# Kernel optimization log

Hardware: AMD Instinct MI355X
Metric: run time of the kernel (lower is better)

Reference implementation:

```python
import jax, jax.numpy as jnp
import numpy as np

N = 20000; DEG = 32; E = N * DEG; F = 142; D = 32; H = 4; HD = H * D; C = 2
_BN = np.float32(1.0 / np.sqrt(1.0 + 1e-5))  # eval-mode BatchNorm1d with running mean 0 / var 1


def _prelu(x, a):
    return jnp.where(x >= 0, x, a * x)


def _layernorm(x, g, b):
    m = x.mean(-1, keepdims=True)
    v = x.var(-1, keepdims=True)
    return (x - m) / jnp.sqrt(v + 1e-5) * g + b


def _conv(h, src, dst, Wq, bq, Wk, bk, Wv, bv, Ws, bs, Wg, bg, lng, lnb, a):
    # TransformerConv: u_dot_v attention (q from src, k from dst), edge softmax over
    # incoming edges of each dst node, u_mul_e + sum aggregation, gated skip, LN, PReLU.
    n = h.shape[0]
    q = (h @ Wq + bq).reshape(n, H, D)
    k = (h @ Wk + bk).reshape(n, H, D)
    v = (h @ Wv + bv).reshape(n, H, D)
    scores = jnp.einsum('ehd,ehd->eh', q[src], k[dst]) / np.float32(np.sqrt(D))  # [E,H]
    m = jax.ops.segment_max(scores, dst, num_segments=n)
    p = jnp.exp(scores - m[dst])
    s = jax.ops.segment_sum(p, dst, num_segments=n)
    sa = p / s[dst]                                                              # [E,H]
    agg = jax.ops.segment_sum(v[src] * sa[..., None], dst, num_segments=n)       # [N,H,D]
    agg = agg.reshape(n, HD)
    skip = h @ Ws + bs
    g = jax.nn.sigmoid(jnp.concatenate([skip, agg, skip - agg], -1) @ Wg + bg)
    rst = g * skip + (1.0 - g) * agg
    return _prelu(_layernorm(rst, lng, lnb), a)


def setup_inputs() -> dict:
    ks = jax.random.split(jax.random.key(0), 64)
    def nrm(i, shape, s=0.05):
        return (jax.random.normal(ks[i], shape) * s).astype(jnp.float32)
    inp = {}
    inp['features'] = jax.random.normal(ks[0], (N, F), jnp.float32)
    inp['label_emb'] = nrm(1, (C + 1, F)).at[C].set(0.0)  # padding_idx = n_classes
    inp['W1'] = nrm(2, (F, HD)); inp['b1'] = jnp.zeros(HD)
    inp['W2'] = nrm(3, (F, HD)); inp['b2'] = jnp.zeros(HD)
    inp['bn0_g'] = jnp.ones(HD); inp['bn0_b'] = jnp.zeros(HD)
    inp['a3'] = 0.25 * jnp.ones(1)
    inp['W3'] = nrm(4, (HD, F)); inp['b3'] = jnp.zeros(F)
    i = 5
    for l, fin in enumerate([F, HD]):
        inp[f'Wq{l}'] = nrm(i, (fin, HD)); i += 1
        inp[f'bq{l}'] = jnp.zeros(HD)
        inp[f'Wk{l}'] = nrm(i, (fin, HD)); i += 1
        inp[f'bk{l}'] = jnp.zeros(HD)
        inp[f'Wv{l}'] = nrm(i, (fin, HD)); i += 1
        inp[f'bv{l}'] = jnp.zeros(HD)
        inp[f'Ws{l}'] = nrm(i, (fin, HD)); i += 1
        inp[f'bs{l}'] = jnp.zeros(HD)
        inp[f'Wg{l}'] = nrm(i, (3 * HD, 1)); i += 1
        inp[f'bg{l}'] = jnp.zeros(1)
        inp[f'ln{l}_g'] = jnp.ones(HD)
        inp[f'ln{l}_b'] = jnp.zeros(HD)
    inp['a_conv'] = 0.25 * jnp.ones(1)  # single PReLU instance shared by both conv layers
    inp['W4'] = nrm(i, (HD, HD)); i += 1; inp['b4'] = jnp.zeros(HD)
    inp['bn1_g'] = jnp.ones(HD); inp['bn1_b'] = jnp.zeros(HD)
    inp['a5'] = 0.25 * jnp.ones(1)
    inp['W5'] = nrm(i, (HD, C)); i += 1; inp['b5'] = jnp.zeros(C)
    inp['labels'] = jax.random.randint(ks[40], (N,), 0, C + 1)
    inp['edge_src'] = jax.random.randint(ks[41], (E,), 0, N)
    inp['edge_dst'] = jnp.repeat(jnp.arange(N), DEG)  # every node has in-degree DEG
    return inp


def reference(features, label_emb, W1, b1, W2, b2, bn0_g, bn0_b, a3, W3, b3,
              Wq0, bq0, Wk0, bk0, Wv0, bv0, Ws0, bs0, Wg0, bg0, ln0_g, ln0_b,
              Wq1, bq1, Wk1, bk1, Wv1, bv1, Ws1, bs1, Wg1, bg1, ln1_g, ln1_b,
              a_conv, W4, b4, bn1_g, bn1_b, a5, W5, b5,
              labels, edge_src, edge_dst):
    le = label_emb[labels]                                   # [N,F]
    le = features @ W1 + b1 + le @ W2 + b2                   # [N,HD]
    le = _prelu(le * _BN * bn0_g + bn0_b, a3) @ W3 + b3      # BN -> PReLU -> Linear
    h = features + le
    h = _conv(h, edge_src, edge_dst, Wq0, bq0, Wk0, bk0, Wv0, bv0, Ws0, bs0, Wg0, bg0, ln0_g, ln0_b, a_conv)
    h = _conv(h, edge_src, edge_dst, Wq1, bq1, Wk1, bk1, Wv1, bv1, Ws1, bs1, Wg1, bg1, ln1_g, ln1_b, a_conv)
    x = h @ W4 + b4
    x = _prelu(x * _BN * bn1_g + bn1_b, a5)
    return x @ W5 + b5                                       # [N, n_classes]
```

## Files before the change

kernel.cpp:

```cpp
#include <hip/hip_runtime.h>
#include <math.h>

#define N_NODES 20000
#define DEG 32
#define F_IN 142
#define HD 128
#define NHEAD 4
#define DHEAD 32
#define N_CLS 2

#define BN_SCALE 0.9999950000374997f
#define INV_SQRT_D 0.17677669529663687f

typedef short v8s __attribute__((ext_vector_type(8)));
typedef float v4f __attribute__((ext_vector_type(4)));

__device__ __forceinline__ unsigned short f2bf(float f) {
    unsigned u = __float_as_uint(f);
    return (unsigned short)((u + 0x7fffu + ((u >> 16) & 1u)) >> 16);
}
__device__ __forceinline__ unsigned pack2bf(float a, float b) {
    return (unsigned)f2bf(a) | ((unsigned)f2bf(b) << 16);
}
__device__ __forceinline__ float bf2f(unsigned short s) {
    return __uint_as_float((unsigned)s << 16);
}
__device__ __forceinline__ float bflo(unsigned u) { return __uint_as_float(u << 16); }
__device__ __forceinline__ float bfhi(unsigned u) { return __uint_as_float(u & 0xffff0000u); }

__device__ __forceinline__ v8s pack8(float4 f0, float4 f1) {
    union { v8s s; unsigned u[4]; } x;
    x.u[0] = pack2bf(f0.x, f0.y);
    x.u[1] = pack2bf(f0.z, f0.w);
    x.u[2] = pack2bf(f1.x, f1.y);
    x.u[3] = pack2bf(f1.z, f1.w);
    return x.s;
}

__device__ __forceinline__ void swizTile(const float* __restrict__ W, int K, int KC,
                                         int tile, int L, short* __restrict__ outBase) {
    const int kc = tile % KC, nt = tile / KC;
    const int n = nt * 16 + (L & 15);
    const int kb = kc * 32 + (L >> 4) * 8;
    short v[8] __attribute__((aligned(16)));
    #pragma unroll
    for (int j = 0; j < 8; ++j) {
        int k = kb + j;
        v[j] = (k < K) ? (short)f2bf(W[(size_t)k * HD + n]) : (short)0;
    }
    *(uint4*)(outBase + ((size_t)tile * 64 + L) * 8) = *(const uint4*)v;
}

__global__ __launch_bounds__(128) void kPrep(
        const float* W142a, const float* W142b, const float* W142c,
        const float* W142d, const float* W142e,
        const float* W128a, const float* W128b, const float* W128c,
        const float* W128d, const float* W128e,
        const float* __restrict__ W3,
        const float* __restrict__ lemb, const float* __restrict__ W2,
        const float* __restrict__ b1, const float* __restrict__ b2,
        short* __restrict__ Wf142, short* __restrict__ Wf128,
        short* __restrict__ W3f, float* __restrict__ E) {
    const int b = blockIdx.x;
    const int t = threadIdx.x;
    if (b < 100) {
        const float* Wt[5] = {W142a, W142b, W142c, W142d, W142e};
        const int idx = b * 2 + (t >> 6);
        const int mat = idx / 40, tile = idx - mat * 40;
        swizTile(Wt[mat], F_IN, 5, tile, t & 63, Wf142 + (size_t)mat * 20480);
    } else if (b < 180) {
        const float* Wt[5] = {W128a, W128b, W128c, W128d, W128e};
        const int idx = (b - 100) * 2 + (t >> 6);
        const int mat = idx >> 5, tile = idx & 31;
        swizTile(Wt[mat], HD, 4, tile, t & 63, Wf128 + (size_t)mat * 16384);
    } else if (b < 198) {
        const int tile = (b - 180) * 2 + (t >> 6);
        const int kc = tile & 3, nt = tile >> 2;
        const int L = t & 63;
        const int n = nt * 16 + (L & 15);
        const int kb = kc * 32 + (L >> 4) * 8;
        short v[8] __attribute__((aligned(16)));
        #pragma unroll
        for (int j = 0; j < 8; ++j)
            v[j] = (n < F_IN) ? (short)f2bf(W3[(size_t)(kb + j) * F_IN + n]) : (short)0;
        *(uint4*)(W3f + ((size_t)tile * 64 + L) * 8) = *(const uint4*)v;
    } else {
        __shared__ float sl[F_IN];
        const int l = b - 198;
        for (int f = t; f < F_IN; f += 128) sl[f] = lemb[l * F_IN + f];
        __syncthreads();
        float acc = b1[t] + b2[t];
        for (int f = 0; f < F_IN; ++f) acc += sl[f] * W2[f * HD + t];
        E[l * HD + t] = acc;
    }
}

__global__ __launch_bounds__(256) void kAB_m(const float* __restrict__ feat,
        const short* __restrict__ W1f, const short* __restrict__ W3f,
        const int* __restrict__ labels, const float* __restrict__ E,
        const float* __restrict__ bng, const float* __restrict__ bnb,
        const float* __restrict__ a3, const float* __restrict__ b3,
        float* __restrict__ h) {
    __shared__ float4 sAv[32 * 164 / 4];
    __shared__ uint4  sTv[32 * 136 / 8];
    __shared__ int sLab[32];
    float* sA = (float*)sAv;
    unsigned short* sT = (unsigned short*)sTv;
    const int tid = threadIdx.x;
    const int row0 = blockIdx.x * 32;
    for (int idx = tid; idx < 32 * F_IN; idx += 256) {
        int r = idx / F_IN, c = idx - r * F_IN;
        sA[r * 164 + c] = feat[(size_t)(row0 + r) * F_IN + c];
    }
    {   const int ZC = 160 - F_IN;
        for (int idx = tid; idx < 32 * ZC; idx += 256) {
            int r = idx / ZC, c = idx - r * ZC;
            sA[r * 164 + F_IN + c] = 0.f;
        }
    }
    if (tid < 32) sLab[tid] = labels[row0 + tid];
    __syncthreads();

    const int lane = tid & 63, w = tid >> 6;
    const int m = lane & 15, q = lane >> 4;
    const int nt0 = w * 2, nt1 = nt0 + 1;

    v4f acc00 = {0.f,0.f,0.f,0.f}, acc01 = acc00, acc10 = acc00, acc11 = acc00;
    #pragma unroll
    for (int kc = 0; kc < 5; ++kc) {
        const float* r0 = sA + m * 164 + kc * 32 + q * 8;
        const float* r1 = sA + (16 + m) * 164 + kc * 32 + q * 8;
        v8s a0 = pack8(*(const float4*)r0, *(const float4*)(r0 + 4));
        v8s a1 = pack8(*(const float4*)r1, *(const float4*)(r1 + 4));
        v8s b0 = *(const v8s*)(W1f + ((size_t)((nt0 * 5 + kc) * 64 + lane)) * 8);
        v8s b1 = *(const v8s*)(W1f + ((size_t)((nt1 * 5 + kc) * 64 + lane)) * 8);
        acc00 = __builtin_amdgcn_mfma_f32_16x16x32_bf16(a0, b0, acc00, 0, 0, 0);
        acc01 = __builtin_amdgcn_mfma_f32_16x16x32_bf16(a0, b1, acc01, 0, 0, 0);
        acc10 = __builtin_amdgcn_mfma_f32_16x16x32_bf16(a1, b0, acc10, 0, 0, 0);
        acc11 = __builtin_amdgcn_mfma_f32_16x16x32_bf16(a1, b1, acc11, 0, 0, 0);
    }
    const int c0 = w * 32 + m, c1 = c0 + 16;
    {
        const float g0 = bng[c0] * BN_SCALE, g1 = bng[c1] * BN_SCALE;
        const float bb0 = bnb[c0], bb1 = bnb[c1];
        const float al = a3[0];
        #pragma unroll
        for (int rt = 0; rt < 2; ++rt) {
            v4f A0 = rt ? acc10 : acc00;
            v4f A1 = rt ? acc11 : acc01;
            #pragma unroll
            for (int i = 0; i < 4; ++i) {
                const int r = rt * 16 + q * 4 + i;
                const int lab = sLab[r];
                float y0 = (A0[i] + E[lab * HD + c0]) * g0 + bb0;
                float y1 = (A1[i] + E[lab * HD + c1]) * g1 + bb1;
                y0 = (y0 >= 0.f) ? y0 : al * y0;
                y1 = (y1 >= 0.f) ? y1 : al * y1;
                sT[r * 136 + c0] = f2bf(y0);
                sT[r * 136 + c1] = f2bf(y1);
            }
        }
    }
    __syncthreads();

    v4f d00 = {0.f,0.f,0.f,0.f}, d01 = d00, d10 = d00, d11 = d00, e0 = d00, e1 = d00;
    #pragma unroll
    for (int kc = 0; kc < 4; ++kc) {
        v8s a0 = *(const v8s*)(sT + m * 136 + kc * 32 + q * 8);
        v8s a1 = *(const v8s*)(sT + (16 + m) * 136 + kc * 32 + q * 8);
        v8s b0 = *(const v8s*)(W3f + ((size_t)((nt0 * 4 + kc) * 64 + lane)) * 8);
        v8s b1 = *(const v8s*)(W3f + ((size_t)((nt1 * 4 + kc) * 64 + lane)) * 8);
        d00 = __builtin_amdgcn_mfma_f32_16x16x32_bf16(a0, b0, d00, 0, 0, 0);
        d01 = __builtin_amdgcn_mfma_f32_16x16x32_bf16(a0, b1, d01, 0, 0, 0);
        d10 = __builtin_amdgcn_mfma_f32_16x16x32_bf16(a1, b0, d10, 0, 0, 0);
        d11 = __builtin_amdgcn_mfma_f32_16x16x32_bf16(a1, b1, d11, 0, 0, 0);
        if (w == 3) {
            v8s b2 = *(const v8s*)(W3f + ((size_t)((8 * 4 + kc) * 64 + lane)) * 8);
            e0 = __builtin_amdgcn_mfma_f32_16x16x32_bf16(a0, b2, e0, 0, 0, 0);
            e1 = __builtin_amdgcn_mfma_f32_16x16x32_bf16(a1, b2, e1, 0, 0, 0);
        }
    }
    const float b30 = b3[c0], b31 = b3[c1];
    #pragma unroll
    for (int rt = 0; rt < 2; ++rt) {
        v4f D0 = rt ? d10 : d00;
        v4f D1 = rt ? d11 : d01;
        #pragma unroll
        for (int i = 0; i < 4; ++i) {
            const int r = row0 + rt * 16 + q * 4 + i;
            h[(size_t)r * F_IN + c0] = feat[(size_t)r * F_IN + c0] + D0[i] + b30;
            h[(size_t)r * F_IN + c1] = feat[(size_t)r * F_IN + c1] + D1[i] + b31;
        }
    }
    if (w == 3) {
        const int c2 = 128 + m;
        if (c2 < F_IN) {
            const float b32 = b3[c2];
            #pragma unroll
            for (int i = 0; i < 4; ++i) {
                const int ra = row0 + q * 4 + i;
                const int rb = ra + 16;
                h[(size_t)ra * F_IN + c2] = feat[(size_t)ra * F_IN + c2] + e0[i] + b32;
                h[(size_t)rb * F_IN + c2] = feat[(size_t)rb * F_IN + c2] + e1[i] + b32;
            }
        }
    }
}

template<int K, int LDSK, int KC>
__global__ __launch_bounds__(256) void kC4_mf(const float* __restrict__ A,
        const short* __restrict__ WfBase,
        const float* __restrict__ bq, const float* __restrict__ bk,
        const float* __restrict__ bv, const float* __restrict__ bs,
        unsigned short* __restrict__ qh, unsigned short* __restrict__ kh,
        unsigned short* __restrict__ vh, float* __restrict__ sOut) {
    __shared__ float4 sAv[32 * LDSK / 4];
    float* sA = (float*)sAv;
    const int tid = threadIdx.x;
    const int row0 = blockIdx.x * 32;
    for (int idx = tid; idx < 32 * K; idx += 256) {
        int r = idx / K, c = idx - r * K;
        sA[r * LDSK + c] = A[(size_t)(row0 + r) * K + c];
    }
    if (K < KC * 32) {
        const int ZC = KC * 32 - K;
        for (int idx = tid; idx < 32 * ZC; idx += 256) {
            int r = idx / ZC, c = idx - r * ZC;
            sA[r * LDSK + K + c] = 0.f;
        }
    }
    __syncthreads();

    const int lane = tid & 63, w = tid >> 6;
    const int m = lane & 15, q = lane >> 4;
    const int nt0 = w * 2, nt1 = nt0 + 1;

    v8s afr0[KC], afr1[KC];
    #pragma unroll
    for (int kc = 0; kc < KC; ++kc) {
        const float* r0 = sA + m * LDSK + kc * 32 + q * 8;
        const float* r1 = sA + (16 + m) * LDSK + kc * 32 + q * 8;
        afr0[kc] = pack8(*(const float4*)r0, *(const float4*)(r0 + 4));
        afr1[kc] = pack8(*(const float4*)r1, *(const float4*)(r1 + 4));
    }

    const int c0 = w * 32 + m, c1 = c0 + 16;
    #pragma unroll
    for (int mat = 0; mat < 4; ++mat) {
        const short* Wf = WfBase + (size_t)mat * (KC * 4096);
        const float* bias = (mat == 0) ? bq : (mat == 1) ? bk : (mat == 2) ? bv : bs;
        v4f acc00 = {0.f,0.f,0.f,0.f}, acc01 = acc00, acc10 = acc00, acc11 = acc00;
        #pragma unroll
        for (int kc = 0; kc < KC; ++kc) {
            v8s b0 = *(const v8s*)(Wf + ((size_t)((nt0 * KC + kc) * 64 + lane)) * 8);
            v8s b1 = *(const v8s*)(Wf + ((size_t)((nt1 * KC + kc) * 64 + lane)) * 8);
            acc00 = __builtin_amdgcn_mfma_f32_16x16x32_bf16(afr0[kc], b0, acc00, 0, 0, 0);
            acc01 = __builtin_amdgcn_mfma_f32_16x16x32_bf16(afr0[kc], b1, acc01, 0, 0, 0);
            acc10 = __builtin_amdgcn_mfma_f32_16x16x32_bf16(afr1[kc], b0, acc10, 0, 0, 0);
            acc11 = __builtin_amdgcn_mfma_f32_16x16x32_bf16(afr1[kc], b1, acc11, 0, 0, 0);
        }
        const float b0v = bias[c0], b1v = bias[c1];
        if (mat < 3) {
            unsigned short* outh = (mat == 0) ? qh : (mat == 1) ? kh : vh;
            unsigned short* outw = outh + ((size_t)w * N_NODES + row0) * DHEAD;
            #pragma unroll
            for (int rt = 0; rt < 2; ++rt) {
                v4f A0 = rt ? acc10 : acc00;
                v4f A1 = rt ? acc11 : acc01;
                #pragma unroll
                for (int i = 0; i < 4; ++i) {
                    const int r = rt * 16 + q * 4 + i;
                    outw[(size_t)r * DHEAD + m]      = f2bf(A0[i] + b0v);
                    outw[(size_t)r * DHEAD + 16 + m] = f2bf(A1[i] + b1v);
                }
            }
        } else {
            #pragma unroll
            for (int rt = 0; rt < 2; ++rt) {
                v4f A0 = rt ? acc10 : acc00;
                v4f A1 = rt ? acc11 : acc01;
                #pragma unroll
                for (int i = 0; i < 4; ++i) {
                    const int r = rt * 16 + q * 4 + i;
                    sOut[(size_t)(row0 + r) * HD + c0] = A0[i] + b0v;
                    sOut[(size_t)(row0 + r) * HD + c1] = A1[i] + b1v;
                }
            }
        }
    }
}

__global__ __launch_bounds__(256) void kD_h(const unsigned short* __restrict__ qh,
        const unsigned short* __restrict__ kh, const unsigned short* __restrict__ vh,
        const int* __restrict__ esrc, float* __restrict__ agg) {
    __shared__ float sk[8][DHEAD];
    __shared__ int ssrc[8][DEG];
    __shared__ float sa[8][DEG];
    const int h = blockIdx.y;
    const int n0 = blockIdx.x * 8;
    const int t = threadIdx.x;
    const int j = t >> 5, e = t & 31;

    ssrc[j][e] = esrc[n0 * DEG + t];
    if (t < 128) {
        unsigned u = *((const unsigned*)(kh + ((size_t)h * N_NODES + n0) * DHEAD) + t);
        float* skf = &sk[0][0];
        skf[2 * t]     = bflo(u);
        skf[2 * t + 1] = bfhi(u);
    }
    __syncthreads();

    const int src = ssrc[j][e];
    const uint4* qp = (const uint4*)(qh + ((size_t)h * N_NODES + src) * DHEAD);
    const float* kj = sk[j];
    float sc = 0.f;
    #pragma unroll
    for (int i = 0; i < 4; ++i) {
        uint4 u = qp[i];
        sc = fmaf(bflo(u.x), kj[i * 8 + 0], sc);
        sc = fmaf(bfhi(u.x), kj[i * 8 + 1], sc);
        sc = fmaf(bflo(u.y), kj[i * 8 + 2], sc);
        sc = fmaf(bfhi(u.y), kj[i * 8 + 3], sc);
        sc = fmaf(bflo(u.z), kj[i * 8 + 4], sc);
        sc = fmaf(bfhi(u.z), kj[i * 8 + 5], sc);
        sc = fmaf(bflo(u.w), kj[i * 8 + 6], sc);
        sc = fmaf(bfhi(u.w), kj[i * 8 + 7], sc);
    }
    sc *= INV_SQRT_D;
    float m = sc;
    #pragma unroll
    for (int off = 16; off > 0; off >>= 1)
        m = fmaxf(m, __shfl_xor(m, off, 32));
    float p = expf(sc - m);
    float ssum = p;
    #pragma unroll
    for (int off = 16; off > 0; off >>= 1)
        ssum += __shfl_xor(ssum, off, 32);
    sa[j][e] = p / ssum;
    __syncthreads();

    const int d = t & 31;
    const unsigned short* vbase = vh + (size_t)h * N_NODES * DHEAD + d;
    float acc = 0.f;
    #pragma unroll
    for (int e2 = 0; e2 < DEG; ++e2) {
        const int s2 = ssrc[j][e2];
        acc = fmaf(bf2f(vbase[(size_t)s2 * DHEAD]), sa[j][e2], acc);
    }
    agg[(size_t)(n0 + j) * HD + h * DHEAD + d] = acc;
}

__device__ __forceinline__ float blockSum128(float v, float* s2, int tid) {
    #pragma unroll
    for (int o = 32; o > 0; o >>= 1) v += __shfl_xor(v, o, 64);
    if ((tid & 63) == 0) s2[tid >> 6] = v;
    __syncthreads();
    float r = s2[0] + s2[1];
    __syncthreads();
    return r;
}

__global__ void kE(const float* __restrict__ skip, const float* __restrict__ agg,
                   const float* __restrict__ Wg, const float* __restrict__ bg,
                   const float* __restrict__ lng, const float* __restrict__ lnb,
                   const float* __restrict__ ac,
                   float* __restrict__ hout) {
    __shared__ float red[2];
    int n = blockIdx.x, c = threadIdx.x;
    float sk = skip[n * HD + c], ag = agg[n * HD + c];
    float part = sk * Wg[c] + ag * Wg[HD + c] + (sk - ag) * Wg[2 * HD + c];
    float z = blockSum128(part, red, c) + bg[0];
    float g = 1.f / (1.f + expf(-z));
    float r = g * sk + (1.f - g) * ag;
    float mean = blockSum128(r, red, c) * (1.f / HD);
    float dv = r - mean;
    float var = blockSum128(dv * dv, red, c) * (1.f / HD);
    float y = dv * rsqrtf(var + 1e-5f) * lng[c] + lnb[c];
    float a = ac[0];
    hout[n * HD + c] = (y >= 0.f) ? y : a * y;
}

__global__ __launch_bounds__(256) void kF_mf2(const float* __restrict__ A,
        const short* __restrict__ W4f, const float* __restrict__ b4,
        const float* __restrict__ bng, const float* __restrict__ bnb,
        const float* __restrict__ a5, const float* __restrict__ W5,
        const float* __restrict__ b5, float* __restrict__ out) {
    __shared__ float4 sAv[32 * 132 / 4];
    float* sA = (float*)sAv;
    const int tid = threadIdx.x;
    const int row0 = blockIdx.x * 32;
    for (int idx = tid; idx < 32 * HD; idx += 256) {
        int r = idx >> 7, c = idx & 127;
        sA[r * 132 + c] = A[(size_t)(row0 + r) * HD + c];
    }
    __syncthreads();
    const int lane = tid & 63, w = tid >> 6;
    const int m = lane & 15, q = lane >> 4;
    const int nt0 = w * 2, nt1 = nt0 + 1;
    v4f acc00 = {0.f,0.f,0.f,0.f}, acc01 = acc00, acc10 = acc00, acc11 = acc00;
    #pragma unroll
    for (int kc = 0; kc < 4; ++kc) {
        const float* r0 = sA + m * 132 + kc * 32 + q * 8;
        const float* r1 = sA + (16 + m) * 132 + kc * 32 + q * 8;
        v8s a0 = pack8(*(const float4*)r0, *(const float4*)(r0 + 4));
        v8s a1 = pack8(*(const float4*)r1, *(const float4*)(r1 + 4));
        v8s b0 = *(const v8s*)(W4f + ((size_t)((nt0 * 4 + kc) * 64 + lane)) * 8);
        v8s b1 = *(const v8s*)(W4f + ((size_t)((nt1 * 4 + kc) * 64 + lane)) * 8);
        acc00 = __builtin_amdgcn_mfma_f32_16x16x32_bf16(a0, b0, acc00, 0, 0, 0);
        acc01 = __builtin_amdgcn_mfma_f32_16x16x32_bf16(a0, b1, acc01, 0, 0, 0);
        acc10 = __builtin_amdgcn_mfma_f32_16x16x32_bf16(a1, b0, acc10, 0, 0, 0);
        acc11 = __builtin_amdgcn_mfma_f32_16x16x32_bf16(a1, b1, acc11, 0, 0, 0);
    }
    __syncthreads();
    const int c0 = w * 32 + m, c1 = c0 + 16;
    const float g0 = bng[c0] * BN_SCALE, g1 = bng[c1] * BN_SCALE;
    const float bb0 = bnb[c0], bb1 = bnb[c1];
    const float b40 = b4[c0], b41 = b4[c1];
    const float al = a5[0];
    #pragma unroll
    for (int rt = 0; rt < 2; ++rt) {
        v4f A0 = rt ? acc10 : acc00;
        v4f A1 = rt ? acc11 : acc01;
        #pragma unroll
        for (int i = 0; i < 4; ++i) {
            const int r = rt * 16 + q * 4 + i;
            float y0 = (A0[i] + b40) * g0 + bb0;
            float y1 = (A1[i] + b41) * g1 + bb1;
            y0 = (y0 >= 0.f) ? y0 : al * y0;
            y1 = (y1 >= 0.f) ? y1 : al * y1;
            sA[r * 132 + c0] = y0;
            sA[r * 132 + c1] = y1;
        }
    }
    __syncthreads();
    if (tid < 64) {
        const int r = tid >> 1, cls = tid & 1;
        const float* yr = sA + r * 132;
        float s = b5[cls];
        #pragma unroll 8
        for (int c = 0; c < HD; ++c)
            s = fmaf(yr[c], W5[c * 2 + cls], s);
        out[(size_t)(row0 + r) * N_CLS + cls] = s;
    }
}

extern "C" void kernel_launch(void* const* d_in, const int* in_sizes, int n_in,
                              void* d_out, int out_size, void* d_ws, size_t ws_size,
                              hipStream_t stream) {
    const float* feat  = (const float*)d_in[0];
    const float* lemb  = (const float*)d_in[1];
    const float* W1    = (const float*)d_in[2];
    const float* b1    = (const float*)d_in[3];
    const float* W2    = (const float*)d_in[4];
    const float* b2    = (const float*)d_in[5];
    const float* bn0g  = (const float*)d_in[6];
    const float* bn0b  = (const float*)d_in[7];
    const float* a3    = (const float*)d_in[8];
    const float* W3    = (const float*)d_in[9];
    const float* b3    = (const float*)d_in[10];
    const float* aconv = (const float*)d_in[35];
    const float* W4    = (const float*)d_in[36];
    const float* b4    = (const float*)d_in[37];
    const float* bn1g  = (const float*)d_in[38];
    const float* bn1b  = (const float*)d_in[39];
    const float* a5    = (const float*)d_in[40];
    const float* W5    = (const float*)d_in[41];
    const float* b5    = (const float*)d_in[42];
    const int*   labels = (const int*)d_in[43];
    const int*   esrc   = (const int*)d_in[44];

    char* ws = (char*)d_ws;
    float* bh  = (float*)ws;                       ws += sizeof(float) * N_NODES * F_IN;
    float* bs  = (float*)ws;                       ws += sizeof(float) * N_NODES * HD;
    float* bag = (float*)ws;                       ws += sizeof(float) * N_NODES * HD;
    float* bh2 = (float*)ws;                       ws += sizeof(float) * N_NODES * HD;
    unsigned short* bqh = (unsigned short*)ws;     ws += sizeof(short) * N_NODES * HD;
    unsigned short* bkh = (unsigned short*)ws;     ws += sizeof(short) * N_NODES * HD;
    unsigned short* bvh = (unsigned short*)ws;     ws += sizeof(short) * N_NODES * HD;
    short* Wf142 = (short*)ws;                     ws += sizeof(short) * 5 * 20480;
    short* Wf128 = (short*)ws;                     ws += sizeof(short) * 5 * 16384;
    short* W3f = (short*)ws;                       ws += sizeof(short) * 36 * 512;
    float* bE  = (float*)ws;                       ws += sizeof(float) * 3 * HD;
    float* out = (float*)d_out;

    dim3 gT(N_NODES / 32);
    dim3 gD(N_NODES / 8, NHEAD);

    kPrep<<<dim3(201), 128, 0, stream>>>(
        W1, (const float*)d_in[11], (const float*)d_in[13],
        (const float*)d_in[15], (const float*)d_in[17],
        (const float*)d_in[23], (const float*)d_in[25],
        (const float*)d_in[27], (const float*)d_in[29], W4,
        W3, lemb, W2, b1, b2,
        Wf142, Wf128, W3f, bE);

    kAB_m<<<gT, 256, 0, stream>>>(feat, Wf142, W3f, labels, bE, bn0g, bn0b, a3, b3, bh);

    kC4_mf<F_IN, 164, 5><<<gT, 256, 0, stream>>>(bh, Wf142 + 20480,
        (const float*)d_in[12], (const float*)d_in[14],
        (const float*)d_in[16], (const float*)d_in[18],
        bqh, bkh, bvh, bs);
    kD_h<<<gD, 256, 0, stream>>>(bqh, bkh, bvh, esrc, bag);
    kE<<<dim3(N_NODES), HD, 0, stream>>>(bs, bag, (const float*)d_in[19], (const float*)d_in[20],
        (const float*)d_in[21], (const float*)d_in[22], aconv, bh2);

    kC4_mf<HD, 132, 4><<<gT, 256, 0, stream>>>(bh2, Wf128,
        (const float*)d_in[24], (const float*)d_in[26],
        (const float*)d_in[28], (const float*)d_in[30],
        bqh, bkh, bvh, bs);
    kD_h<<<gD, 256, 0, stream>>>(bqh, bkh, bvh, esrc, bag);
    kE<<<dim3(N_NODES), HD, 0, stream>>>(bs, bag, (const float*)d_in[31], (const float*)d_in[32],
        (const float*)d_in[33], (const float*)d_in[34], aconv, bh2);

    kF_mf2<<<gT, 256, 0, stream>>>(bh2, Wf128 + 4 * 16384, b4, bn1g, bn1b, a5, W5, b5, out);
}
```

Before: 313.7 us.

## Fuse input MLP with first QKV projection and gate/LN into following GEMMs

```diff
diff --git a/kernel.cpp b/kernel.cpp
--- a/kernel.cpp
+++ b/kernel.cpp
@@ -95,17 +95,22 @@
     }
 }
 
-__global__ __launch_bounds__(256) void kAB_m(const float* __restrict__ feat,
-        const short* __restrict__ W1f, const short* __restrict__ W3f,
+__global__ __launch_bounds__(256) void kABC(const float* __restrict__ feat,
+        const short* __restrict__ Wf142, const short* __restrict__ W3f,
         const int* __restrict__ labels, const float* __restrict__ E,
         const float* __restrict__ bng, const float* __restrict__ bnb,
         const float* __restrict__ a3, const float* __restrict__ b3,
-        float* __restrict__ h) {
+        const float* __restrict__ bq, const float* __restrict__ bk,
+        const float* __restrict__ bv, const float* __restrict__ bsb,
+        unsigned short* __restrict__ qh, unsigned short* __restrict__ kh,
+        unsigned short* __restrict__ vh, float* __restrict__ sOut) {
     __shared__ float4 sAv[32 * 164 / 4];
     __shared__ uint4  sTv[32 * 136 / 8];
+    __shared__ uint4  sHv[32 * 168 / 8];
     __shared__ int sLab[32];
     float* sA = (float*)sAv;
     unsigned short* sT = (unsigned short*)sTv;
+    unsigned short* sH = (unsigned short*)sHv;
     const int tid = threadIdx.x;
     const int row0 = blockIdx.x * 32;
     for (int idx = tid; idx < 32 * F_IN; idx += 256) {
@@ -124,23 +129,23 @@
     const int lane = tid & 63, w = tid >> 6;
     const int m = lane & 15, q = lane >> 4;
     const int nt0 = w * 2, nt1 = nt0 + 1;
-
-    v4f acc00 = {0.f,0.f,0.f,0.f}, acc01 = acc00, acc10 = acc00, acc11 = acc00;
-    #pragma unroll
-    for (int kc = 0; kc < 5; ++kc) {
-        const float* r0 = sA + m * 164 + kc * 32 + q * 8;
-        const float* r1 = sA + (16 + m) * 164 + kc * 32 + q * 8;
-        v8s a0 = pack8(*(const float4*)r0, *(const float4*)(r0 + 4));
-        v8s a1 = pack8(*(const float4*)r1, *(const float4*)(r1 + 4));
-        v8s b0 = *(const v8s*)(W1f + ((size_t)((nt0 * 5 + kc) * 64 + lane)) * 8);
-        v8s b1 = *(const v8s*)(W1f + ((size_t)((nt1 * 5 + kc) * 64 + lane)) * 8);
-        acc00 = __builtin_amdgcn_mfma_f32_16x16x32_bf16(a0, b0, acc00, 0, 0, 0);
-        acc01 = __builtin_amdgcn_mfma_f32_16x16x32_bf16(a0, b1, acc01, 0, 0, 0);
-        acc10 = __builtin_amdgcn_mfma_f32_16x16x32_bf16(a1, b0, acc10, 0, 0, 0);
-        acc11 = __builtin_amdgcn_mfma_f32_16x16x32_bf16(a1, b1, acc11, 0, 0, 0);
-    }
     const int c0 = w * 32 + m, c1 = c0 + 16;
+
     {
+        v4f acc00 = {0.f,0.f,0.f,0.f}, acc01 = acc00, acc10 = acc00, acc11 = acc00;
+        #pragma unroll
+        for (int kc = 0; kc < 5; ++kc) {
+            const float* r0 = sA + m * 164 + kc * 32 + q * 8;
+            const float* r1 = sA + (16 + m) * 164 + kc * 32 + q * 8;
+            v8s a0 = pack8(*(const float4*)r0, *(const float4*)(r0 + 4));
+            v8s a1 = pack8(*(const float4*)r1, *(const float4*)(r1 + 4));
+            v8s b0 = *(const v8s*)(Wf142 + ((size_t)((nt0 * 5 + kc) * 64 + lane)) * 8);
+            v8s b1 = *(const v8s*)(Wf142 + ((size_t)((nt1 * 5 + kc) * 64 + lane)) * 8);
+            acc00 = __builtin_amdgcn_mfma_f32_16x16x32_bf16(a0, b0, acc00, 0, 0, 0);
+            acc01 = __builtin_amdgcn_mfma_f32_16x16x32_bf16(a0, b1, acc01, 0, 0, 0);
+            acc10 = __builtin_amdgcn_mfma_f32_16x16x32_bf16(a1, b0, acc10, 0, 0, 0);
+            acc11 = __builtin_amdgcn_mfma_f32_16x16x32_bf16(a1, b1, acc11, 0, 0, 0);
+        }
         const float g0 = bng[c0] * BN_SCALE, g1 = bng[c1] * BN_SCALE;
         const float bb0 = bnb[c0], bb1 = bnb[c1];
         const float al = a3[0];
@@ -163,97 +168,197 @@
     }
     __syncthreads();
 
-    v4f d00 = {0.f,0.f,0.f,0.f}, d01 = d00, d10 = d00, d11 = d00, e0 = d00, e1 = d00;
-    #pragma unroll
-    for (int kc = 0; kc < 4; ++kc) {
-        v8s a0 = *(const v8s*)(sT + m * 136 + kc * 32 + q * 8);
-        v8s a1 = *(const v8s*)(sT + (16 + m) * 136 + kc * 32 + q * 8);
-        v8s b0 = *(const v8s*)(W3f + ((size_t)((nt0 * 4 + kc) * 64 + lane)) * 8);
-        v8s b1 = *(const v8s*)(W3f + ((size_t)((nt1 * 4 + kc) * 64 + lane)) * 8);
-        d00 = __builtin_amdgcn_mfma_f32_16x16x32_bf16(a0, b0, d00, 0, 0, 0);
-        d01 = __builtin_amdgcn_mfma_f32_16x16x32_bf16(a0, b1, d01, 0, 0, 0);
-        d10 = __builtin_amdgcn_mfma_f32_16x16x32_bf16(a1, b0, d10, 0, 0, 0);
-        d11 = __builtin_amdgcn_mfma_f32_16x16x32_bf16(a1, b1, d11, 0, 0, 0);
+    {
+        v4f d00 = {0.f,0.f,0.f,0.f}, d01 = d00, d10 = d00, d11 = d00, e0 = d00, e1 = d00;
+        #pragma unroll
+        for (int kc = 0; kc < 4; ++kc) {
+            v8s a0 = *(const v8s*)(sT + m * 136 + kc * 32 + q * 8);
+            v8s a1 = *(const v8s*)(sT + (16 + m) * 136 + kc * 32 + q * 8);
+            v8s b0 = *(const v8s*)(W3f + ((size_t)((nt0 * 4 + kc) * 64 + lane)) * 8);
+            v8s b1 = *(const v8s*)(W3f + ((size_t)((nt1 * 4 + kc) * 64 + lane)) * 8);
+            d00 = __builtin_amdgcn_mfma_f32_16x16x32_bf16(a0, b0, d00, 0, 0, 0);
+            d01 = __builtin_amdgcn_mfma_f32_16x16x32_bf16(a0, b1, d01, 0, 0, 0);
+            d10 = __builtin_amdgcn_mfma_f32_16x16x32_bf16(a1, b0, d10, 0, 0, 0);
+            d11 = __builtin_amdgcn_mfma_f32_16x16x32_bf16(a1, b1, d11, 0, 0, 0);
+            if (w == 3) {
+                v8s b2 = *(const v8s*)(W3f + ((size_t)((8 * 4 + kc) * 64 + lane)) * 8);
+                e0 = __builtin_amdgcn_mfma_f32_16x16x32_bf16(a0, b2, e0, 0, 0, 0);
+                e1 = __builtin_amdgcn_mfma_f32_16x16x32_bf16(a1, b2, e1, 0, 0, 0);
+            }
+        }
+        const float b30 = b3[c0], b31 = b3[c1];
+        #pragma unroll
+        for (int rt = 0; rt < 2; ++rt) {
+            v4f D0 = rt ? d10 : d00;
+            v4f D1 = rt ? d11 : d01;
+            #pragma unroll
+            for (int i = 0; i < 4; ++i) {
+                const int r = rt * 16 + q * 4 + i;
+                sH[r * 168 + c0] = f2bf(sA[r * 164 + c0] + D0[i] + b30);
+                sH[r * 168 + c1] = f2bf(sA[r * 164 + c1] + D1[i] + b31);
+            }
+        }
         if (w == 3) {
-            v8s b2 = *(const v8s*)(W3f + ((size_t)((8 * 4 + kc) * 64 + lane)) * 8);
-            e0 = __builtin_amdgcn_mfma_f32_16x16x32_bf16(a0, b2, e0, 0, 0, 0);
-            e1 = __builtin_amdgcn_mfma_f32_16x16x32_bf16(a1, b2, e1, 0, 0, 0);
-        }
-    }
-    const float b30 = b3[c0], b31 = b3[c1];
-    #pragma unroll
-    for (int rt = 0; rt < 2; ++rt) {
-        v4f D0 = rt ? d10 : d00;
-        v4f D1 = rt ? d11 : d01;
-        #pragma unroll
-        for (int i = 0; i < 4; ++i) {
-            const int r = row0 + rt * 16 + q * 4 + i;
-            h[(size_t)r * F_IN + c0] = feat[(size_t)r * F_IN + c0] + D0[i] + b30;
-            h[(size_t)r * F_IN + c1] = feat[(size_t)r * F_IN + c1] + D1[i] + b31;
-        }
-    }
-    if (w == 3) {
-        const int c2 = 128 + m;
-        if (c2 < F_IN) {
-            const float b32 = b3[c2];
+            const int c2 = 128 + m;
+            const bool ok = (c2 < F_IN);
+            const float b32 = ok ? b3[c2] : 0.f;
             #pragma unroll
             for (int i = 0; i < 4; ++i) {
-                const int ra = row0 + q * 4 + i;
+                const int ra = q * 4 + i;
                 const int rb = ra + 16;
-                h[(size_t)ra * F_IN + c2] = feat[(size_t)ra * F_IN + c2] + e0[i] + b32;
-                h[(size_t)rb * F_IN + c2] = feat[(size_t)rb * F_IN + c2] + e1[i] + b32;
-            }
-        }
-    }
-}
-
-template<int K, int LDSK, int KC>
-__global__ __launch_bounds__(256) void kC4_mf(const float* __restrict__ A,
-        const short* __restrict__ WfBase,
+                sH[ra * 168 + c2] = ok ? f2bf(sA[ra * 164 + c2] + e0[i] + b32) : (unsigned short)0;
+                sH[rb * 168 + c2] = ok ? f2bf(sA[rb * 164 + c2] + e1[i] + b32) : (unsigned short)0;
+            }
+        }
+        if (tid < 256) {
+            const int r = tid >> 3, cp = tid & 7;
+            ((unsigned*)sH)[r * 84 + 72 + cp] = 0u;
+        }
+    }
+    __syncthreads();
+
+    v8s afr0[5], afr1[5];
+    #pragma unroll
+    for (int kc = 0; kc < 5; ++kc) {
+        afr0[kc] = *(const v8s*)(sH + m * 168 + kc * 32 + q * 8);
+        afr1[kc] = *(const v8s*)(sH + (16 + m) * 168 + kc * 32 + q * 8);
+    }
+    #pragma unroll
+    for (int mat = 0; mat < 4; ++mat) {
+        const short* Wf = Wf142 + (size_t)(mat + 1) * 20480;
+        const float* bias = (mat == 0) ? bq : (mat == 1) ? bk : (mat == 2) ? bv : bsb;
+        v4f acc00 = {0.f,0.f,0.f,0.f}, acc01 = acc00, acc10 = acc00, acc11 = acc00;
+        #pragma unroll
+        for (int kc = 0; kc < 5; ++kc) {
+            v8s b0 = *(const v8s*)(Wf + ((size_t)((nt0 * 5 + kc) * 64 + lane)) * 8);
+            v8s b1 = *(const v8s*)(Wf + ((size_t)((nt1 * 5 + kc) * 64 + lane)) * 8);
+            acc00 = __builtin_amdgcn_mfma_f32_16x16x32_bf16(afr0[kc], b0, acc00, 0, 0, 0);
+            acc01 = __builtin_amdgcn_mfma_f32_16x16x32_bf16(afr0[kc], b1, acc01, 0, 0, 0);
+            acc10 = __builtin_amdgcn_mfma_f32_16x16x32_bf16(afr1[kc], b0, acc10, 0, 0, 0);
+            acc11 = __builtin_amdgcn_mfma_f32_16x16x32_bf16(afr1[kc], b1, acc11, 0, 0, 0);
+        }
+        const float b0v = bias[c0], b1v = bias[c1];
+        if (mat < 3) {
+            unsigned short* outh = (mat == 0) ? qh : (mat == 1) ? kh : vh;
+            unsigned short* outw = outh + ((size_t)w * N_NODES + row0) * DHEAD;
+            #pragma unroll
+            for (int rt = 0; rt < 2; ++rt) {
+                v4f A0 = rt ? acc10 : acc00;
+                v4f A1 = rt ? acc11 : acc01;
+                #pragma unroll
+                for (int i = 0; i < 4; ++i) {
+                    const int r = rt * 16 + q * 4 + i;
+                    outw[(size_t)r * DHEAD + m]      = f2bf(A0[i] + b0v);
+                    outw[(size_t)r * DHEAD + 16 + m] = f2bf(A1[i] + b1v);
+                }
+            }
+        } else {
+            #pragma unroll
+            for (int rt = 0; rt < 2; ++rt) {
+                v4f A0 = rt ? acc10 : acc00;
+                v4f A1 = rt ? acc11 : acc01;
+                #pragma unroll
+                for (int i = 0; i < 4; ++i) {
+                    const int r = rt * 16 + q * 4 + i;
+                    sOut[(size_t)(row0 + r) * HD + c0] = A0[i] + b0v;
+                    sOut[(size_t)(row0 + r) * HD + c1] = A1[i] + b1v;
+                }
+            }
+        }
+    }
+}
+
+__device__ __forceinline__ void kE_phase(const float* __restrict__ skip,
+        const float* __restrict__ agg, const float* __restrict__ Wg,
+        const float* __restrict__ bg, const float* __restrict__ lng,
+        const float* __restrict__ lnb, const float* __restrict__ ac,
+        float* sA, int row0, int t) {
+    const int e = t & 31, g8 = t >> 5;
+    const float al = ac[0];
+    const float bg0 = bg[0];
+    for (int ng = 0; ng < 4; ++ng) {
+        const int j = ng * 8 + g8;
+        const size_t n = (size_t)(row0 + j);
+        float skv[4], agv[4];
+        float part = 0.f;
+        #pragma unroll
+        for (int k2 = 0; k2 < 4; ++k2) {
+            const int c = e + 32 * k2;
+            skv[k2] = skip[n * HD + c];
+            agv[k2] = agg[n * HD + c];
+            part += skv[k2] * Wg[c] + agv[k2] * Wg[HD + c] + (skv[k2] - agv[k2]) * Wg[2 * HD + c];
+        }
+        #pragma unroll
+        for (int off = 16; off > 0; off >>= 1)
+            part += __shfl_xor(part, off, 32);
+        const float g = 1.f / (1.f + expf(-(part + bg0)));
+        float rv[4], rsum = 0.f;
+        #pragma unroll
+        for (int k2 = 0; k2 < 4; ++k2) {
+            rv[k2] = g * skv[k2] + (1.f - g) * agv[k2];
+            rsum += rv[k2];
+        }
+        #pragma unroll
+        for (int off = 16; off > 0; off >>= 1)
+            rsum += __shfl_xor(rsum, off, 32);
+        const float mean = rsum * (1.f / HD);
+        float dv[4], vsum = 0.f;
+        #pragma unroll
+        for (int k2 = 0; k2 < 4; ++k2) {
+            dv[k2] = rv[k2] - mean;
+            vsum += dv[k2] * dv[k2];
+        }
+        #pragma unroll
+        for (int off = 16; off > 0; off >>= 1)
+            vsum += __shfl_xor(vsum, off, 32);
+        const float inv = rsqrtf(vsum * (1.f / HD) + 1e-5f);
+        #pragma unroll
+        for (int k2 = 0; k2 < 4; ++k2) {
+            const int c = e + 32 * k2;
+            float y = dv[k2] * inv * lng[c] + lnb[c];
+            sA[j * 132 + c] = (y >= 0.f) ? y : al * y;
+        }
+    }
+}
+
+__global__ __launch_bounds__(256) void kEC4(const float* __restrict__ skip,
+        const float* __restrict__ agg,
+        const float* __restrict__ Wg, const float* __restrict__ bg,
+        const float* __restrict__ lng, const float* __restrict__ lnb,
+        const float* __restrict__ ac,
+        const short* __restrict__ Wf128,
         const float* __restrict__ bq, const float* __restrict__ bk,
-        const float* __restrict__ bv, const float* __restrict__ bs,
+        const float* __restrict__ bv, const float* __restrict__ bsb,
         unsigned short* __restrict__ qh, unsigned short* __restrict__ kh,
         unsigned short* __restrict__ vh, float* __restrict__ sOut) {
-    __shared__ float4 sAv[32 * LDSK / 4];
+    __shared__ float4 sAv[32 * 132 / 4];
     float* sA = (float*)sAv;
     const int tid = threadIdx.x;
     const int row0 = blockIdx.x * 32;
-    for (int idx = tid; idx < 32 * K; idx += 256) {
-        int r = idx / K, c = idx - r * K;
-        sA[r * LDSK + c] = A[(size_t)(row0 + r) * K + c];
-    }
-    if (K < KC * 32) {
-        const int ZC = KC * 32 - K;
-        for (int idx = tid; idx < 32 * ZC; idx += 256) {
-            int r = idx / ZC, c = idx - r * ZC;
-            sA[r * LDSK + K + c] = 0.f;
-        }
-    }
+    kE_phase(skip, agg, Wg, bg, lng, lnb, ac, sA, row0, tid);
     __syncthreads();
 
     const int lane = tid & 63, w = tid >> 6;
     const int m = lane & 15, q = lane >> 4;
     const int nt0 = w * 2, nt1 = nt0 + 1;
-
-    v8s afr0[KC], afr1[KC];
-    #pragma unroll
-    for (int kc = 0; kc < KC; ++kc) {
-        const float* r0 = sA + m * LDSK + kc * 32 + q * 8;
-        const float* r1 = sA + (16 + m) * LDSK + kc * 32 + q * 8;
+    v8s afr0[4], afr1[4];
+    #pragma unroll
+    for (int kc = 0; kc < 4; ++kc) {
+        const float* r0 = sA + m * 132 + kc * 32 + q * 8;
+        const float* r1 = sA + (16 + m) * 132 + kc * 32 + q * 8;
         afr0[kc] = pack8(*(const float4*)r0, *(const float4*)(r0 + 4));
         afr1[kc] = pack8(*(const float4*)r1, *(const float4*)(r1 + 4));
     }
-
     const int c0 = w * 32 + m, c1 = c0 + 16;
     #pragma unroll
     for (int mat = 0; mat < 4; ++mat) {
-        const short* Wf = WfBase + (size_t)mat * (KC * 4096);
-        const float* bias = (mat == 0) ? bq : (mat == 1) ? bk : (mat == 2) ? bv : bs;
+        const short* Wf = Wf128 + (size_t)mat * 16384;
+        const float* bias = (mat == 0) ? bq : (mat == 1) ? bk : (mat == 2) ? bv : bsb;
         v4f acc00 = {0.f,0.f,0.f,0.f}, acc01 = acc00, acc10 = acc00, acc11 = acc00;
         #pragma unroll
-        for (int kc = 0; kc < KC; ++kc) {
-            v8s b0 = *(const v8s*)(Wf + ((size_t)((nt0 * KC + kc) * 64 + lane)) * 8);
-            v8s b1 = *(const v8s*)(Wf + ((size_t)((nt1 * KC + kc) * 64 + lane)) * 8);
+        for (int kc = 0; kc < 4; ++kc) {
+            v8s b0 = *(const v8s*)(Wf + ((size_t)((nt0 * 4 + kc) * 64 + lane)) * 8);
+            v8s b1 = *(const v8s*)(Wf + ((size_t)((nt1 * 4 + kc) * 64 + lane)) * 8);
             acc00 = __builtin_amdgcn_mfma_f32_16x16x32_bf16(afr0[kc], b0, acc00, 0, 0, 0);
             acc01 = __builtin_amdgcn_mfma_f32_16x16x32_bf16(afr0[kc], b1, acc01, 0, 0, 0);
             acc10 = __builtin_amdgcn_mfma_f32_16x16x32_bf16(afr1[kc], b0, acc10, 0, 0, 0);
@@ -350,37 +455,11 @@
     agg[(size_t)(n0 + j) * HD + h * DHEAD + d] = acc;
 }
 
-__device__ __forceinline__ float blockSum128(float v, float* s2, int tid) {
-    #pragma unroll
-    for (int o = 32; o > 0; o >>= 1) v += __shfl_xor(v, o, 64);
-    if ((tid & 63) == 0) s2[tid >> 6] = v;
-    __syncthreads();
-    float r = s2[0] + s2[1];
-    __syncthreads();
-    return r;
-}
-
-__global__ void kE(const float* __restrict__ skip, const float* __restrict__ agg,
-                   const float* __restrict__ Wg, const float* __restrict__ bg,
-                   const float* __restrict__ lng, const float* __restrict__ lnb,
-                   const float* __restrict__ ac,
-                   float* __restrict__ hout) {
-    __shared__ float red[2];
-    int n = blockIdx.x, c = threadIdx.x;
-    float sk = skip[n * HD + c], ag = agg[n * HD + c];
-    float part = sk * Wg[c] + ag * Wg[HD + c] + (sk - ag) * Wg[2 * HD + c];
-    float z = blockSum128(part, red, c) + bg[0];
-    float g = 1.f / (1.f + expf(-z));
-    float r = g * sk + (1.f - g) * ag;
-    float mean = blockSum128(r, red, c) * (1.f / HD);
-    float dv = r - mean;
-    float var = blockSum128(dv * dv, red, c) * (1.f / HD);
-    float y = dv * rsqrtf(var + 1e-5f) * lng[c] + lnb[c];
-    float a = ac[0];
-    hout[n * HD + c] = (y >= 0.f) ? y : a * y;
-}
-
-__global__ __launch_bounds__(256) void kF_mf2(const float* __restrict__ A,
+__global__ __launch_bounds__(256) void kEF(const float* __restrict__ skip,
+        const float* __restrict__ agg,
+        const float* __restrict__ Wg, const float* __restrict__ bg,
+        const float* __restrict__ lng, const float* __restrict__ lnb,
+        const float* __restrict__ ac,
         const short* __restrict__ W4f, const float* __restrict__ b4,
         const float* __restrict__ bng, const float* __restrict__ bnb,
         const float* __restrict__ a5, const float* __restrict__ W5,
@@ -389,11 +468,9 @@
     float* sA = (float*)sAv;
     const int tid = threadIdx.x;
     const int row0 = blockIdx.x * 32;
-    for (int idx = tid; idx < 32 * HD; idx += 256) {
-        int r = idx >> 7, c = idx & 127;
-        sA[r * 132 + c] = A[(size_t)(row0 + r) * HD + c];
-    }
-    __syncthreads();
+    kE_phase(skip, agg, Wg, bg, lng, lnb, ac, sA, row0, tid);
+    __syncthreads();
+
     const int lane = tid & 63, w = tid >> 6;
     const int m = lane & 15, q = lane >> 4;
     const int nt0 = w * 2, nt1 = nt0 + 1;
@@ -470,10 +547,8 @@
     const int*   esrc   = (const int*)d_in[44];
 
     char* ws = (char*)d_ws;
-    float* bh  = (float*)ws;                       ws += sizeof(float) * N_NODES * F_IN;
     float* bs  = (float*)ws;                       ws += sizeof(float) * N_NODES * HD;
     float* bag = (float*)ws;                       ws += sizeof(float) * N_NODES * HD;
-    float* bh2 = (float*)ws;                       ws += sizeof(float) * N_NODES * HD;
     unsigned short* bqh = (unsigned short*)ws;     ws += sizeof(short) * N_NODES * HD;
     unsigned short* bkh = (unsigned short*)ws;     ws += sizeof(short) * N_NODES * HD;
     unsigned short* bvh = (unsigned short*)ws;     ws += sizeof(short) * N_NODES * HD;
@@ -494,23 +569,23 @@
         W3, lemb, W2, b1, b2,
         Wf142, Wf128, W3f, bE);
 
-    kAB_m<<<gT, 256, 0, stream>>>(feat, Wf142, W3f, labels, bE, bn0g, bn0b, a3, b3, bh);
-
-    kC4_mf<F_IN, 164, 5><<<gT, 256, 0, stream>>>(bh, Wf142 + 20480,
+    kABC<<<gT, 256, 0, stream>>>(feat, Wf142, W3f, labels, bE, bn0g, bn0b, a3, b3,
         (const float*)d_in[12], (const float*)d_in[14],
         (const float*)d_in[16], (const float*)d_in[18],
         bqh, bkh, bvh, bs);
     kD_h<<<gD, 256, 0, stream>>>(bqh, bkh, bvh, esrc, bag);
-    kE<<<dim3(N_NODES), HD, 0, stream>>>(bs, bag, (const float*)d_in[19], (const float*)d_in[20],
-        (const float*)d_in[21], (const float*)d_in[22], aconv, bh2);
-
-    kC4_mf<HD, 132, 4><<<gT, 256, 0, stream>>>(bh2, Wf128,
+
+    kEC4<<<gT, 256, 0, stream>>>(bs, bag,
+        (const float*)d_in[19], (const float*)d_in[20],
+        (const float*)d_in[21], (const float*)d_in[22], aconv,
+        Wf128,
         (const float*)d_in[24], (const float*)d_in[26],
         (const float*)d_in[28], (const float*)d_in[30],
         bqh, bkh, bvh, bs);
     kD_h<<<gD, 256, 0, stream>>>(bqh, bkh, bvh, esrc, bag);
-    kE<<<dim3(N_NODES), HD, 0, stream>>>(bs, bag, (const float*)d_in[31], (const float*)d_in[32],
-        (const float*)d_in[33], (const float*)d_in[34], aconv, bh2);
-
-    kF_mf2<<<gT, 256, 0, stream>>>(bh2, Wf128 + 4 * 16384, b4, bn1g, bn1b, a5, W5, b5, out);
-}
+
+    kEF<<<gT, 256, 0, stream>>>(bs, bag,
+        (const float*)d_in[31], (const float*)d_in[32],
+        (const float*)d_in[33], (const float*)d_in[34], aconv,
+        Wf128 + 4 * 16384, b4, bn1g, bn1b, a5, W5, b5, out);
+}
```

New measurement: 280.7 us. 1.12x faster.
